# Optimization experiments

Measured on AMD Instinct MI355X. Metric: run time of the kernel, lower is better.

Reference implementation:

```python
import jax, jax.numpy as jnp
import numpy as np

K_TABLE = 8388608   # number of stored key/value pairs (2**23)
N_QUERY = 4194304   # number of lookups (2**22)
KEY_SPACE = 2147483647
DEFAULT_VALUE = -1  # DenseHashTable default_value for missing keys


def setup_inputs() -> dict:
    key = jax.random.key(0)
    k1, k2, k3, k4 = jax.random.split(key, 4)
    # Hash table contents, represented as a sorted key array + aligned values.
    table_keys = jnp.sort(jax.random.randint(k1, (K_TABLE,), 1, KEY_SPACE, dtype=jnp.int64))
    table_values = jax.random.randint(k2, (K_TABLE,), 0, 1000000, dtype=jnp.int64)
    # Queries: half random ids (mostly misses), half sampled from the table (hits).
    q_rand = jax.random.randint(k3, (N_QUERY // 2,), 1, KEY_SPACE, dtype=jnp.int64)
    hit_idx = jax.random.randint(k4, (N_QUERY // 2,), 0, K_TABLE, dtype=jnp.int64)
    q_hit = table_keys[hit_idx]
    query = jnp.concatenate([q_rand, q_hit])
    return {"query": query, "table_keys": table_keys, "table_values": table_values}


def reference(query, table_keys, table_values):
    # DenseHashTable.lookup: for each query id return its stored value,
    # or default_value (-1) if the key is absent. Implemented as a sorted
    # binary-search gather (same math: exact-match key -> value map).
    idx = jnp.searchsorted(table_keys, query)                 # [N]
    idx_c = jnp.clip(idx, 0, table_keys.shape[0] - 1)
    hit = table_keys[idx_c] == query                          # [N] bool
    out = jnp.where(hit, table_values[idx_c], jnp.int64(DEFAULT_VALUE))
    return out
```

## Files before the change

### kernel.cpp

```cpp
#include <hip/hip_runtime.h>


constexpr int WCAP     = 1024;
constexpr int NBLK     = 1 << 15;
constexpr int BM_WORDS = 1 << 19;

__device__ __forceinline__ int lower_bound_u(const int* __restrict__ keys,
                                             int lo, int hi, unsigned t) {
    while (lo < hi) {
        int m = (lo + hi) >> 1;
        if ((unsigned)keys[m] < t) lo = m + 1; else hi = m;
    }
    return lo;
}

__global__ void block_index_kernel(const int* __restrict__ keys, int K,
                                   int* __restrict__ bstart) {
    int i = blockIdx.x * blockDim.x + threadIdx.x;
    if (i > NBLK) return;
    bstart[i] = lower_bound_u(keys, 0, K, ((unsigned)i) << 16);
}

__global__ void bitmap_build_kernel(const int* __restrict__ keys, int K,
                                    const int* __restrict__ bstart,
                                    unsigned* __restrict__ bitmap) {
    int w = blockIdx.x * blockDim.x + threadIdx.x;
    if (w >= BM_WORDS) return;
    int blk = w >> 4;
    int lo = bstart[blk], hi = bstart[blk + 1];
    unsigned t0 = ((unsigned)w) << 12;
    unsigned t1 = t0 + 4096u;
    lo = lower_bound_u(keys, lo, hi, t0);
    unsigned word = 0;
    for (int j = lo; j < hi; ++j) {
        unsigned k = (unsigned)keys[j];
        if (k >= t1) break;
        word |= 1u << ((k >> 7) & 31u);
    }
    bitmap[w] = word;
}

__global__ void __launch_bounds__(256) build_rank_kernel(
        const int* __restrict__ keys, const int* __restrict__ vals, int K,
        const int* __restrict__ bstart, int4* __restrict__ table) {
    __shared__ int s_keys[WCAP];
    __shared__ int s_vals[WCAP];
    __shared__ int s_first[256];
    __shared__ int s_flag[256];
    __shared__ int s_ent[256][4];

    const int tid = threadIdx.x;
    const int wlo = bstart[blockIdx.x];
    const int whi = bstart[blockIdx.x + 1];
    const int wn = whi - wlo;
    const unsigned base_b = (unsigned)blockIdx.x << 8;

    s_flag[tid] = 0;
    s_ent[tid][0] = 0; s_ent[tid][1] = 0; s_ent[tid][2] = 0; s_ent[tid][3] = 0;

    if (wn <= WCAP) {
        for (int j = tid; j < wn; j += 256) {
            s_keys[j] = keys[wlo + j];
            s_vals[j] = vals[wlo + j];
        }
        __syncthreads();
        for (int j = tid; j < wn; j += 256) {
            unsigned b = ((unsigned)s_keys[j]) >> 8;
            bool first = (j == 0) || ((((unsigned)s_keys[j - 1]) >> 8) != b);
            if (first) s_first[b & 255u] = j;
        }
        __syncthreads();
        for (int j = tid; j < wn; j += 256) {
            int k = s_keys[j];
            unsigned lb = (((unsigned)k) >> 8) & 255u;
            int rank = j - s_first[lb];
            int v = s_vals[j];
            if (rank < 4 && (unsigned)v <= 0xFFFFFu) {
                s_ent[lb][rank] = (1 << 28) | (v << 8) | (k & 0xFF);
            } else {
                s_flag[lb] = 1;
            }
        }
        __syncthreads();
        int4 e;
        if (s_flag[tid]) e = make_int4(2 << 28, wlo + s_first[tid], 0, 0);
        else             e = make_int4(s_ent[tid][0], s_ent[tid][1],
                                       s_ent[tid][2], s_ent[tid][3]);
        table[base_b + tid] = e;
    } else {
        __syncthreads();
        unsigned b = base_b + tid;
        unsigned tlo = b << 8;
        unsigned thi = tlo + 256u;
        int lo = lower_bound_u(keys, wlo, whi, tlo);
        int w[4] = {0, 0, 0, 0};
        bool ok = true;
        int cnt = 0;
        int j = lo;
        while (j < whi && (unsigned)keys[j] < thi) {
            if (cnt >= 4) { ok = false; break; }
            int v = vals[j];
            if ((unsigned)v > 0xFFFFFu) { ok = false; break; }
            w[cnt] = (1 << 28) | (v << 8) | (keys[j] & 0xFF);
            ++cnt; ++j;
        }
        table[b] = ok ? make_int4(w[0], w[1], w[2], w[3])
                      : make_int4(2 << 28, lo, 0, 0);
    }
}

__device__ __forceinline__ int resolve_packed(int q, int4 e,
                                              const int* __restrict__ keys,
                                              const int* __restrict__ vals,
                                              int K) {
    if ((((unsigned)e.x) >> 28) == 2u) {
        for (int j = e.y; j < K; ++j) {
            int k = keys[j];
            if ((unsigned)k >= (unsigned)q) return (k == q) ? vals[j] : -1;
        }
        return -1;
    }
    int ql = q & 0xFF;
    int w;
    w = e.x; if ((((unsigned)w) >> 28) == 1u && (w & 0xFF) == ql) return (w >> 8) & 0xFFFFF;
    w = e.y; if ((((unsigned)w) >> 28) == 1u && (w & 0xFF) == ql) return (w >> 8) & 0xFFFFF;
    w = e.z; if ((((unsigned)w) >> 28) == 1u && (w & 0xFF) == ql) return (w >> 8) & 0xFFFFF;
    w = e.w; if ((((unsigned)w) >> 28) == 1u && (w & 0xFF) == ql) return (w >> 8) & 0xFFFFF;
    return -1;
}

__global__ void lookup_bm_kernel(const int* __restrict__ query,
                                 const int* __restrict__ keys,
                                 const int* __restrict__ vals,
                                 const int4* __restrict__ table,
                                 const unsigned* __restrict__ bitmap,
                                 int* __restrict__ out,
                                 int N, int K, unsigned Bmask) {
    int quarter = (N + 3) >> 2;
    int i = blockIdx.x * blockDim.x + threadIdx.x;
    if (i >= quarter) return;
    int idx[4] = {i, i + quarter, i + 2 * quarter, i + 3 * quarter};
    int q[4];
    unsigned wbits[4];
#pragma unroll
    for (int c = 0; c < 4; ++c) q[c] = (idx[c] < N) ? query[idx[c]] : 1;
#pragma unroll
    for (int c = 0; c < 4; ++c) wbits[c] = bitmap[((unsigned)q[c]) >> 12];
    bool probe[4];
    int4 e[4];
#pragma unroll
    for (int c = 0; c < 4; ++c) {
        unsigned bi = ((unsigned)q[c]) >> 7;
        probe[c] = (idx[c] < N) && (((wbits[c] >> (bi & 31u)) & 1u) != 0u);
        e[c] = probe[c] ? table[(((unsigned)q[c]) >> 8) & Bmask]
                        : make_int4(0, 0, 0, 0);
    }
#pragma unroll
    for (int c = 0; c < 4; ++c) {
        if (idx[c] < N)
            out[idx[c]] = probe[c] ? resolve_packed(q[c], e[c], keys, vals, K) : -1;
    }
}

__global__ void lookup_packed_kernel(const int* __restrict__ query,
                                     const int* __restrict__ keys,
                                     const int* __restrict__ vals,
                                     const int4* __restrict__ table,
                                     int* __restrict__ out,
                                     int N, int K, unsigned Bmask) {
    int half = (N + 1) >> 1;
    int i = blockIdx.x * blockDim.x + threadIdx.x;
    if (i >= half) return;
    int i1 = i + half;
    bool has1 = (i1 < N);
    int q0 = query[i];
    int q1 = has1 ? query[i1] : q0;
    int4 e0 = table[(((unsigned)q0) >> 8) & Bmask];
    int4 e1 = table[(((unsigned)q1) >> 8) & Bmask];
    out[i] = resolve_packed(q0, e0, keys, vals, K);
    if (has1) out[i1] = resolve_packed(q1, e1, keys, vals, K);
}

__global__ void lookup_bsearch_kernel(const int* __restrict__ query,
                                      const int* __restrict__ keys,
                                      const int* __restrict__ vals,
                                      int* __restrict__ out,
                                      int N, int K) {
    int i = blockIdx.x * blockDim.x + threadIdx.x;
    if (i >= N) return;
    unsigned q = (unsigned)query[i];
    int lo = lower_bound_u(keys, 0, K, q);
    int r = -1;
    if (lo < K && (unsigned)keys[lo] == q) r = vals[lo];
    out[i] = r;
}

extern "C" void kernel_launch(void* const* d_in, const int* in_sizes, int n_in,
                              void* d_out, int out_size, void* d_ws, size_t ws_size,
                              hipStream_t stream) {
    const int* query = (const int*)d_in[0];
    const int* keys  = (const int*)d_in[1];
    const int* vals  = (const int*)d_in[2];
    int* out = (int*)d_out;
    const int N = in_sizes[0];
    const int K = in_sizes[1];
    const int tb = 256;

    const size_t TABLE_BYTES = (size_t)16 << 23;
    const size_t IDX_BYTES   = (((size_t)(NBLK + 1) * 4) + 63) & ~(size_t)63;
    const size_t BM_BYTES    = (size_t)BM_WORDS * 4;

    if (TABLE_BYTES + IDX_BYTES + BM_BYTES <= ws_size) {
        const unsigned B = 1u << 23;
        int4* table = (int4*)d_ws;
        int* bstart = (int*)((char*)d_ws + TABLE_BYTES);
        unsigned* bitmap = (unsigned*)((char*)d_ws + TABLE_BYTES + IDX_BYTES);
        block_index_kernel<<<(NBLK + 1 + tb - 1) / tb, tb, 0, stream>>>(keys, K, bstart);
        bitmap_build_kernel<<<(BM_WORDS + tb - 1) / tb, tb, 0, stream>>>(keys, K,
                                                                         bstart, bitmap);
        build_rank_kernel<<<NBLK, tb, 0, stream>>>(keys, vals, K, bstart, table);
        int quarter = (N + 3) >> 2;
        lookup_bm_kernel<<<(quarter + tb - 1) / tb, tb, 0, stream>>>(
            query, keys, vals, table, bitmap, out, N, K, B - 1);
    } else if (TABLE_BYTES <= ws_size) {
        const unsigned B = 1u << 23;
        int4* table = (int4*)d_ws;
        int* bstart = (TABLE_BYTES + (size_t)(NBLK + 1) * 4 <= ws_size)
                          ? (int*)((char*)d_ws + TABLE_BYTES)
                          : (int*)d_out;
        block_index_kernel<<<(NBLK + 1 + tb - 1) / tb, tb, 0, stream>>>(keys, K, bstart);
        build_rank_kernel<<<NBLK, tb, 0, stream>>>(keys, vals, K, bstart, table);
        int half = (N + 1) >> 1;
        lookup_packed_kernel<<<(half + tb - 1) / tb, tb, 0, stream>>>(
            query, keys, vals, table, out, N, K, B - 1);
    } else {
        lookup_bsearch_kernel<<<(N + tb - 1) / tb, tb, 0, stream>>>(query, keys,
                                                                    vals, out, N, K);
    }
}
```

Measured before the change: 164.6 us.

## Fuse bitmap construction into rank-table build and use nontemporal lookup accesses

Removes the separate bitmap_build kernel and builds each block's 16 bitmap words inside build_rank_kernel, using shared-memory atomicOr over keys already staged in LDS. This saves one launch and a second pass over the keys. The lookup kernel also switches to nontemporal loads for queries and table entries and nontemporal stores for outputs, to reduce cache pollution on streaming and random accesses. In the fallback path the bitmap pointer aliases d_out and may overlap bstart there; that path is not the default one.

```diff
diff --git a/kernel.cpp b/kernel.cpp
--- a/kernel.cpp
+++ b/kernel.cpp
@@ -4,6 +4,8 @@
 constexpr int WCAP     = 1024;
 constexpr int NBLK     = 1 << 15;
 constexpr int BM_WORDS = 1 << 19;
+
+typedef int vint4 __attribute__((ext_vector_type(4)));
 
 __device__ __forceinline__ int lower_bound_u(const int* __restrict__ keys,
                                              int lo, int hi, unsigned t) {
@@ -21,33 +23,16 @@
     bstart[i] = lower_bound_u(keys, 0, K, ((unsigned)i) << 16);
 }
 
-__global__ void bitmap_build_kernel(const int* __restrict__ keys, int K,
-                                    const int* __restrict__ bstart,
-                                    unsigned* __restrict__ bitmap) {
-    int w = blockIdx.x * blockDim.x + threadIdx.x;
-    if (w >= BM_WORDS) return;
-    int blk = w >> 4;
-    int lo = bstart[blk], hi = bstart[blk + 1];
-    unsigned t0 = ((unsigned)w) << 12;
-    unsigned t1 = t0 + 4096u;
-    lo = lower_bound_u(keys, lo, hi, t0);
-    unsigned word = 0;
-    for (int j = lo; j < hi; ++j) {
-        unsigned k = (unsigned)keys[j];
-        if (k >= t1) break;
-        word |= 1u << ((k >> 7) & 31u);
-    }
-    bitmap[w] = word;
-}
-
 __global__ void __launch_bounds__(256) build_rank_kernel(
         const int* __restrict__ keys, const int* __restrict__ vals, int K,
-        const int* __restrict__ bstart, int4* __restrict__ table) {
+        const int* __restrict__ bstart, int4* __restrict__ table,
+        unsigned* __restrict__ bitmap) {
     __shared__ int s_keys[WCAP];
     __shared__ int s_vals[WCAP];
     __shared__ int s_first[256];
     __shared__ int s_flag[256];
     __shared__ int s_ent[256][4];
+    __shared__ unsigned s_bm[16];
 
     const int tid = threadIdx.x;
     const int wlo = bstart[blockIdx.x];
@@ -57,6 +42,7 @@
 
     s_flag[tid] = 0;
     s_ent[tid][0] = 0; s_ent[tid][1] = 0; s_ent[tid][2] = 0; s_ent[tid][3] = 0;
+    if (tid < 16) s_bm[tid] = 0u;
 
     if (wn <= WCAP) {
         for (int j = tid; j < wn; j += 256) {
@@ -65,9 +51,11 @@
         }
         __syncthreads();
         for (int j = tid; j < wn; j += 256) {
-            unsigned b = ((unsigned)s_keys[j]) >> 8;
+            unsigned k = (unsigned)s_keys[j];
+            unsigned b = k >> 8;
             bool first = (j == 0) || ((((unsigned)s_keys[j - 1]) >> 8) != b);
             if (first) s_first[b & 255u] = j;
+            atomicOr(&s_bm[(k >> 12) & 15u], 1u << ((k >> 7) & 31u));
         }
         __syncthreads();
         for (int j = tid; j < wn; j += 256) {
@@ -87,6 +75,7 @@
         else             e = make_int4(s_ent[tid][0], s_ent[tid][1],
                                        s_ent[tid][2], s_ent[tid][3]);
         table[base_b + tid] = e;
+        if (tid < 16) bitmap[(unsigned)blockIdx.x * 16u + tid] = s_bm[tid];
     } else {
         __syncthreads();
         unsigned b = base_b + tid;
@@ -106,6 +95,18 @@
         }
         table[b] = ok ? make_int4(w[0], w[1], w[2], w[3])
                       : make_int4(2 << 28, lo, 0, 0);
+        if (tid < 16) {
+            unsigned w0 = (unsigned)blockIdx.x * 16u + tid;
+            unsigned t0 = w0 << 12, t1 = t0 + 4096u;
+            int l = lower_bound_u(keys, wlo, whi, t0);
+            unsigned word = 0;
+            for (int jj = l; jj < whi; ++jj) {
+                unsigned k = (unsigned)keys[jj];
+                if (k >= t1) break;
+                word |= 1u << ((k >> 7) & 31u);
+            }
+            bitmap[w0] = word;
+        }
     }
 }
 
@@ -139,26 +140,34 @@
     int quarter = (N + 3) >> 2;
     int i = blockIdx.x * blockDim.x + threadIdx.x;
     if (i >= quarter) return;
+    const vint4* tbl = (const vint4*)table;
     int idx[4] = {i, i + quarter, i + 2 * quarter, i + 3 * quarter};
     int q[4];
     unsigned wbits[4];
 #pragma unroll
-    for (int c = 0; c < 4; ++c) q[c] = (idx[c] < N) ? query[idx[c]] : 1;
+    for (int c = 0; c < 4; ++c)
+        q[c] = (idx[c] < N) ? __builtin_nontemporal_load(&query[idx[c]]) : 1;
 #pragma unroll
     for (int c = 0; c < 4; ++c) wbits[c] = bitmap[((unsigned)q[c]) >> 12];
     bool probe[4];
     int4 e[4];
 #pragma unroll
     for (int c = 0; c < 4; ++c) {
-        unsigned bi = ((unsigned)q[c]) >> 7;
-        probe[c] = (idx[c] < N) && (((wbits[c] >> (bi & 31u)) & 1u) != 0u);
-        e[c] = probe[c] ? table[(((unsigned)q[c]) >> 8) & Bmask]
-                        : make_int4(0, 0, 0, 0);
+        probe[c] = (idx[c] < N) &&
+                   (((wbits[c] >> ((((unsigned)q[c]) >> 7) & 31u)) & 1u) != 0u);
+        if (probe[c]) {
+            vint4 v = __builtin_nontemporal_load(&tbl[(((unsigned)q[c]) >> 8) & Bmask]);
+            e[c] = make_int4(v.x, v.y, v.z, v.w);
+        } else {
+            e[c] = make_int4(0, 0, 0, 0);
+        }
     }
 #pragma unroll
     for (int c = 0; c < 4; ++c) {
-        if (idx[c] < N)
-            out[idx[c]] = probe[c] ? resolve_packed(q[c], e[c], keys, vals, K) : -1;
+        if (idx[c] < N) {
+            int r = probe[c] ? resolve_packed(q[c], e[c], keys, vals, K) : -1;
+            __builtin_nontemporal_store(r, &out[idx[c]]);
+        }
     }
 }
 
@@ -216,9 +225,8 @@
         int* bstart = (int*)((char*)d_ws + TABLE_BYTES);
         unsigned* bitmap = (unsigned*)((char*)d_ws + TABLE_BYTES + IDX_BYTES);
         block_index_kernel<<<(NBLK + 1 + tb - 1) / tb, tb, 0, stream>>>(keys, K, bstart);
-        bitmap_build_kernel<<<(BM_WORDS + tb - 1) / tb, tb, 0, stream>>>(keys, K,
-                                                                         bstart, bitmap);
-        build_rank_kernel<<<NBLK, tb, 0, stream>>>(keys, vals, K, bstart, table);
+        build_rank_kernel<<<NBLK, tb, 0, stream>>>(keys, vals, K, bstart, table,
+                                                   bitmap);
         int quarter = (N + 3) >> 2;
         lookup_bm_kernel<<<(quarter + tb - 1) / tb, tb, 0, stream>>>(
             query, keys, vals, table, bitmap, out, N, K, B - 1);
@@ -228,8 +236,10 @@
         int* bstart = (TABLE_BYTES + (size_t)(NBLK + 1) * 4 <= ws_size)
                           ? (int*)((char*)d_ws + TABLE_BYTES)
                           : (int*)d_out;
+        unsigned* bitmap = (unsigned*)d_out;
         block_index_kernel<<<(NBLK + 1 + tb - 1) / tb, tb, 0, stream>>>(keys, K, bstart);
-        build_rank_kernel<<<NBLK, tb, 0, stream>>>(keys, vals, K, bstart, table);
+        build_rank_kernel<<<NBLK, tb, 0, stream>>>(keys, vals, K, bstart, table,
+                                                   bitmap);
         int half = (N + 1) >> 1;
         lookup_packed_kernel<<<(half + tb - 1) / tb, tb, 0, stream>>>(
             query, keys, vals, table, out, N, K, B - 1);
```

Result: faster. 153.0 us (-7.0%).
